# Kernel optimization log

Measured on AMD Instinct MI355X. Metric: run time of the kernel, lower is better.

Reference implementation:

```python
import jax, jax.numpy as jnp
import numpy as np

D_MODEL = 2048
NUM_HEADS = 16
HEAD_DIM = D_MODEL // NUM_HEADS  # 128; scale uses head_dim even though attention is over full d_model
B, S = 2, 2048


def setup_inputs() -> dict:
    key = jax.random.key(0)
    ks = jax.random.split(key, 5)
    x = jax.random.normal(ks[0], (B, S, D_MODEL), dtype=jnp.float32)
    # causal additive mask, as typically passed to this module (2D, sliced mask[-s:, :kv])
    neg = jnp.float32(-1e9)
    mask = jnp.where(jnp.triu(jnp.ones((S, S), dtype=bool), k=1), neg, jnp.float32(0.0))
    std = 1.0 / np.sqrt(D_MODEL)
    Wq = jax.random.normal(ks[1], (D_MODEL, D_MODEL), dtype=jnp.float32) * std
    Wk = jax.random.normal(ks[2], (D_MODEL, D_MODEL), dtype=jnp.float32) * std
    Wv = jax.random.normal(ks[3], (D_MODEL, D_MODEL), dtype=jnp.float32) * std
    Wo = jax.random.normal(ks[4], (D_MODEL, D_MODEL), dtype=jnp.float32) * std
    return {"x": x, "mask": mask, "Wq": Wq, "Wk": Wk, "Wv": Wv, "Wo": Wo}


def reference(x, mask, Wq, Wk, Wv, Wo):
    # nn.Linear(bias=False): y = x @ W^T
    q = jnp.einsum('bsd,ed->bse', x, Wq)  # [B,S,D]
    k = jnp.einsum('bsd,ed->bse', x, Wk)
    v = jnp.einsum('bsd,ed->bse', x, Wv)
    scale = jnp.float32(HEAD_DIM ** -0.5)
    # NOTE: faithful to source — contraction over full d_model, no head split
    scores = jnp.einsum('bsd,btd->bst', q, k) * scale  # [B,S,S]
    scores = scores + mask  # mask[-s:, :kv] == mask here (s == kv)
    weights = jax.nn.softmax(scores, axis=-1)
    out = jnp.einsum('bst,btd->bsd', weights, v)
    return jnp.einsum('bsd,ed->bse', out, Wo)
```

## Files before the change

### kernel.cpp

```cpp
#include <hip/hip_runtime.h>

#define DM  2048
#define SQ  2048
#define NB  2
#define BSZ (NB * SQ)

typedef _Float16 f16x8 __attribute__((ext_vector_type(8)));
typedef __attribute__((ext_vector_type(4))) float f32x4;

#define ASG(p) (const __attribute__((address_space(1))) void*)(p)
#define ASL(p) (__attribute__((address_space(3))) void*)(p)

__device__ __forceinline__ unsigned short f2h(float f) {
  union { _Float16 h; unsigned short u; } x;
  x.h = (_Float16)f;
  return x.u;
}

__global__ __launch_bounds__(256) void cast_f32(const float4* __restrict__ in,
                                                ushort4* __restrict__ out,
                                                int n4) {
  int i = blockIdx.x * 256 + threadIdx.x;
  if (i >= n4) return;
  float4 v = in[i];
  ushort4 h;
  h.x = f2h(v.x); h.y = f2h(v.y); h.z = f2h(v.z); h.w = f2h(v.w);
  out[i] = h;
}

#define SBAR8() do { \
    __builtin_amdgcn_sched_barrier(0); \
    __builtin_amdgcn_s_barrier(); \
    __builtin_amdgcn_sched_barrier(0); \
  } while (0)

#define STAGE8(BUFL, HALF, T) do { \
    const unsigned short* G_ = ((HALF) < 2) ? Ab : Bb; \
    const int ldG_ = ((HALF) < 2) ? ldA : ldB; \
    const int r0_ = (((HALF) < 2) ? bm0 : bn0) + ((HALF) & 1) * 128; \
    const long k0_ = (long)((T) << 6); \
    char* db_ = ldsb + (BUFL) * 65536 + (HALF) * 16384 + tid * 16; \
    const unsigned short* s0_ = G_ + (long)(r0_ + srow) * ldG_ + k0_ + scsw; \
    const unsigned short* s1_ = G_ + (long)(r0_ + 64 + srow) * ldG_ + k0_ + scsw; \
    __builtin_amdgcn_global_load_lds(ASG(s0_), ASL(db_), 16, 0, 0); \
    __builtin_amdgcn_global_load_lds(ASG(s1_), ASL(db_ + 8192), 16, 0, 0); \
  } while (0)

#define LDA8(BUFL, MQ, Af) do { \
    const char* ba_ = ldsb + (BUFL) * 65536 + wm * 16384 + (MQ) * 8192 + arow; \
    _Pragma("unroll") for (int mm_ = 0; mm_ < 4; mm_++) { \
      Af[mm_][0] = *(const f16x8*)(ba_ + mm_ * 2048 + sl0); \
      Af[mm_][1] = *(const f16x8*)(ba_ + mm_ * 2048 + sl1); } \
  } while (0)

#define LDB8(BUFL, NQ, Bf) do { \
    const char* bb_ = ldsb + (BUFL) * 65536 + 32768 + (wn * 2 + (NQ)) * 4096 + arow; \
    _Pragma("unroll") for (int nn_ = 0; nn_ < 2; nn_++) { \
      Bf[nn_][0] = *(const f16x8*)(bb_ + nn_ * 2048 + sl0); \
      Bf[nn_][1] = *(const f16x8*)(bb_ + nn_ * 2048 + sl1); } \
  } while (0)

#define PH8(Af, Bf, MQ, NQ) do { \
    __builtin_amdgcn_s_setprio(1); \
    _Pragma("unroll") for (int mm_ = 0; mm_ < 4; mm_++) \
    _Pragma("unroll") for (int nn_ = 0; nn_ < 2; nn_++) \
    _Pragma("unroll") for (int ks_ = 0; ks_ < 2; ks_++) \
      acc[(MQ) * 4 + mm_][(NQ) * 2 + nn_] = __builtin_amdgcn_mfma_f32_16x16x32_f16( \
          Af[mm_][ks_], Bf[nn_][ks_], acc[(MQ) * 4 + mm_][(NQ) * 2 + nn_], 0, 0, 0); \
    __builtin_amdgcn_s_setprio(0); \
  } while (0)

#define GROUP8(BUFL, T) do { \
    LDA8(BUFL, 0, a0); LDB8(BUFL, 0, b0); \
    if ((T) + 1 < NT) STAGE8(BUFL ^ 1, 3, (T) + 1); \
    SBAR8(); PH8(a0, b0, 0, 0); SBAR8(); \
    LDA8(BUFL, 1, a1); \
    SBAR8(); PH8(a1, b0, 1, 0); SBAR8(); \
    LDB8(BUFL, 1, b1); \
    if ((T) + 2 < NT) STAGE8(BUFL, 0, (T) + 2); \
    SBAR8(); PH8(a1, b1, 1, 1); SBAR8(); \
    if ((T) + 2 < NT) { STAGE8(BUFL, 1, (T) + 2); STAGE8(BUFL, 2, (T) + 2); } \
    SBAR8(); PH8(a0, b1, 0, 1); \
    __builtin_amdgcn_sched_barrier(0); \
    if ((T) + 1 < NT) { \
      if ((T) + 1 == NT - 1) { asm volatile("s_waitcnt vmcnt(0)" ::: "memory"); } \
      else                   { asm volatile("s_waitcnt vmcnt(6)" ::: "memory"); } \
    } \
    __builtin_amdgcn_s_barrier(); \
    __builtin_amdgcn_sched_barrier(0); \
  } while (0)

template <int OM>
__global__ __launch_bounds__(512, 2) void gemm8p(
    const unsigned short* __restrict__ A, const unsigned short* __restrict__ B,
    float* __restrict__ Cf, unsigned short* __restrict__ Ch,
    int K, int ldA, int ldB, int ldC) {
  __shared__ __align__(16) char ldsarr[131072];
  char* ldsb = ldsarr;

  const int bm0 = blockIdx.x * 256;
  const int bn0 = blockIdx.y * 256;
  const unsigned short* Ab = A;
  const unsigned short* Bb = B;

  const int tid = threadIdx.x, lane = tid & 63, wid = tid >> 6;
  const int wm = wid >> 2, wn = wid & 3;
  const int fr = lane & 15, fq = lane >> 4;
  const int NT = K >> 6;

  const int sl0 = ((fq ^ (fr & 7)) << 4);
  const int sl1 = (((4 + fq) ^ (fr & 7)) << 4);
  const int arow = fr << 7;

  const int srow = tid >> 3;
  const int scsw = ((tid & 7) ^ (srow & 7)) << 3;

  f32x4 acc[8][4];
#pragma unroll
  for (int m = 0; m < 8; m++)
#pragma unroll
    for (int n = 0; n < 4; n++)
#pragma unroll
      for (int r = 0; r < 4; r++) acc[m][n][r] = 0.f;

  f16x8 a0[4][2], a1[4][2], b0[2][2], b1[2][2];

  STAGE8(0, 0, 0); STAGE8(0, 1, 0); STAGE8(0, 2, 0); STAGE8(0, 3, 0);
  STAGE8(1, 0, 1); STAGE8(1, 1, 1); STAGE8(1, 2, 1);
  asm volatile("s_waitcnt vmcnt(6)" ::: "memory");
  __builtin_amdgcn_s_barrier();
  __builtin_amdgcn_sched_barrier(0);

  for (int t = 0; t < NT; t += 2) {
    GROUP8(0, t);
    GROUP8(1, t + 1);
  }

#pragma unroll
  for (int mq = 0; mq < 2; mq++)
#pragma unroll
    for (int mm = 0; mm < 4; mm++)
#pragma unroll
      for (int nq = 0; nq < 2; nq++)
#pragma unroll
        for (int nn = 0; nn < 2; nn++) {
          const int col = bn0 + wn * 64 + nq * 32 + nn * 16 + fr;
#pragma unroll
          for (int r = 0; r < 4; r++) {
            const long row = (long)bm0 + wm * 128 + mq * 64 + mm * 16 + fq * 4 + r;
            const long ci = row * ldC + col;
            if constexpr (OM == 0) Cf[ci] = acc[mq * 4 + mm][nq * 2 + nn][r];
            else                   Ch[ci] = f2h(acc[mq * 4 + mm][nq * 2 + nn][r]);
          }
        }
}

#define STAGER(BUFL, REG, U, T) do { \
    const unsigned short* G_ = (REG) ? Bb : Ab; \
    const int ldG_ = (REG) ? ldB : ldA; \
    const int r0_ = ((REG) ? bn0 : bm0) + (U) * 64; \
    const long k0_ = (long)((T) << 6); \
    char* db_ = ldsb + (BUFL) * 49152 + (REG) * 16384 + (U) * 8192 + tid * 16; \
    const unsigned short* s_ = G_ + (long)(r0_ + srow) * ldG_ + k0_ + scsw; \
    __builtin_amdgcn_global_load_lds(ASG(s_), ASL(db_), 16, 0, 0); \
  } while (0)

#define LDAR(BUFL, MH, Af) do { \
    const char* ba_ = ldsb + (BUFL) * 49152 + (wm * 64 + (MH) * 32) * 128 + arow; \
    _Pragma("unroll") for (int mm_ = 0; mm_ < 2; mm_++) { \
      Af[mm_][0] = *(const f16x8*)(ba_ + mm_ * 2048 + sl0); \
      Af[mm_][1] = *(const f16x8*)(ba_ + mm_ * 2048 + sl1); } \
  } while (0)

#define LDBR(BUFL, NH, Bf) do { \
    const char* bb_ = ldsb + (BUFL) * 49152 + 16384 + (wn * 64 + (NH) * 32) * 128 + arow; \
    _Pragma("unroll") for (int nn_ = 0; nn_ < 2; nn_++) { \
      Bf[nn_][0] = *(const f16x8*)(bb_ + nn_ * 2048 + sl0); \
      Bf[nn_][1] = *(const f16x8*)(bb_ + nn_ * 2048 + sl1); } \
  } while (0)

#define PHR(Af, Bf, MH, NH) do { \
    __builtin_amdgcn_s_setprio(1); \
    _Pragma("unroll") for (int mm_ = 0; mm_ < 2; mm_++) \
    _Pragma("unroll") for (int nn_ = 0; nn_ < 2; nn_++) \
    _Pragma("unroll") for (int ks_ = 0; ks_ < 2; ks_++) \
      acc[(MH) * 2 + mm_][(NH) * 2 + nn_] = __builtin_amdgcn_mfma_f32_16x16x32_f16( \
          Af[mm_][ks_], Bf[nn_][ks_], acc[(MH) * 2 + mm_][(NH) * 2 + nn_], 0, 0, 0); \
    __builtin_amdgcn_s_setprio(0); \
  } while (0)

#define GROUPR(BUFL, T) do { \
    LDAR(BUFL, 0, a0); LDBR(BUFL, 0, b0); \
    if ((T) + 1 < NT) STAGER(BUFL ^ 1, 1, 3, (T) + 1); \
    SBAR8(); PHR(a0, b0, 0, 0); SBAR8(); \
    LDAR(BUFL, 1, a1); \
    SBAR8(); PHR(a1, b0, 1, 0); SBAR8(); \
    LDBR(BUFL, 1, b1); \
    if ((T) + 2 < NT) { STAGER(BUFL, 0, 0, (T) + 2); STAGER(BUFL, 0, 1, (T) + 2); } \
    SBAR8(); PHR(a1, b1, 1, 1); SBAR8(); \
    if ((T) + 2 < NT) { STAGER(BUFL, 1, 0, (T) + 2); STAGER(BUFL, 1, 1, (T) + 2); STAGER(BUFL, 1, 2, (T) + 2); } \
    SBAR8(); PHR(a0, b1, 0, 1); \
    __builtin_amdgcn_sched_barrier(0); \
    if ((T) + 1 < NT) { \
      if ((T) + 1 == NT - 1) { asm volatile("s_waitcnt vmcnt(0)" ::: "memory"); } \
      else                   { asm volatile("s_waitcnt vmcnt(5)" ::: "memory"); } \
    } \
    __builtin_amdgcn_s_barrier(); \
    __builtin_amdgcn_sched_barrier(0); \
  } while (0)

template <int OM, int CAUSAL>
__global__ __launch_bounds__(512, 2) void gemm8pR(
    const unsigned short* __restrict__ A, const unsigned short* __restrict__ B,
    float* __restrict__ Cf, unsigned short* __restrict__ Ch,
    int K, long sAb, long sBb, long sCb,
    int ldA, int ldB, int ldC, float alpha) {
  __shared__ __align__(16) char ldsarr[98304];
  char* ldsb = ldsarr;

  const int bm0 = blockIdx.x * 128;
  const int bn0 = blockIdx.y * 256;
  if (CAUSAL == 1 && bn0 > bm0 + 127) return;

  const int z = blockIdx.z;
  const unsigned short* Ab = A + (long)z * sAb;
  const unsigned short* Bb = B + (long)z * sBb;
  const long cb = (long)z * sCb;

  const int tid = threadIdx.x, lane = tid & 63, wid = tid >> 6;
  const int wm = wid >> 2, wn = wid & 3;
  const int fr = lane & 15, fq = lane >> 4;
  int NT = K >> 6;
  if (CAUSAL == 2) NT = (bm0 + 128) >> 6;

  const int sl0 = ((fq ^ (fr & 7)) << 4);
  const int sl1 = (((4 + fq) ^ (fr & 7)) << 4);
  const int arow = fr << 7;

  const int srow = tid >> 3;
  const int scsw = ((tid & 7) ^ (srow & 7)) << 3;

  f32x4 acc[4][4];
#pragma unroll
  for (int m = 0; m < 4; m++)
#pragma unroll
    for (int n = 0; n < 4; n++)
#pragma unroll
      for (int r = 0; r < 4; r++) acc[m][n][r] = 0.f;

  f16x8 a0[2][2], a1[2][2], b0[2][2], b1[2][2];

  STAGER(0, 0, 0, 0); STAGER(0, 0, 1, 0);
  STAGER(0, 1, 0, 0); STAGER(0, 1, 1, 0); STAGER(0, 1, 2, 0); STAGER(0, 1, 3, 0);
  STAGER(1, 0, 0, 1); STAGER(1, 0, 1, 1);
  STAGER(1, 1, 0, 1); STAGER(1, 1, 1, 1); STAGER(1, 1, 2, 1);
  asm volatile("s_waitcnt vmcnt(5)" ::: "memory");
  __builtin_amdgcn_s_barrier();
  __builtin_amdgcn_sched_barrier(0);

  for (int t = 0; t < NT; t += 2) {
    GROUPR(0, t);
    GROUPR(1, t + 1);
  }

#pragma unroll
  for (int mh = 0; mh < 2; mh++)
#pragma unroll
    for (int mm = 0; mm < 2; mm++)
#pragma unroll
      for (int nh = 0; nh < 2; nh++)
#pragma unroll
        for (int nn = 0; nn < 2; nn++) {
          const int col = bn0 + wn * 64 + nh * 32 + nn * 16 + fr;
#pragma unroll
          for (int r = 0; r < 4; r++) {
            const long row = (long)bm0 + wm * 64 + mh * 32 + mm * 16 + fq * 4 + r;
            const long ci = cb + row * ldC + col;
            const float vv = acc[mh * 2 + mm][nh * 2 + nn][r] * alpha;
            if constexpr (OM == 0) Cf[ci] = vv;
            else                   Ch[ci] = f2h(vv);
          }
        }
}

__global__ __launch_bounds__(256) void softmax_causal(const float* __restrict__ sc,
                                                      unsigned short* __restrict__ pr) {
  const int row = blockIdx.x;
  const int s = row & (SQ - 1);
  const long base = (long)row * SQ;
  const int n = s + 1;
  const int tid = threadIdx.x;
  const int lane = tid & 63;
  const int wv = tid >> 6;
  __shared__ float red[4];

  float v[8];
  float mx = -3.0e38f;
#pragma unroll
  for (int j = 0; j < 8; j++) {
    const int i = tid + j * 256;
    v[j] = (i < n) ? sc[base + i] : -3.0e38f;
    mx = fmaxf(mx, v[j]);
  }
#pragma unroll
  for (int o = 32; o >= 1; o >>= 1) mx = fmaxf(mx, __shfl_xor(mx, o));
  if (lane == 0) red[wv] = mx;
  __syncthreads();
  mx = fmaxf(fmaxf(red[0], red[1]), fmaxf(red[2], red[3]));
  __syncthreads();

  float sum = 0.f;
#pragma unroll
  for (int j = 0; j < 8; j++) {
    const int i = tid + j * 256;
    v[j] = (i < n) ? __expf(v[j] - mx) : 0.f;
    sum += v[j];
  }
#pragma unroll
  for (int o = 32; o >= 1; o >>= 1) sum += __shfl_xor(sum, o);
  if (lane == 0) red[wv] = sum;
  __syncthreads();
  const float inv = 1.f / (red[0] + red[1] + red[2] + red[3]);
#pragma unroll
  for (int j = 0; j < 8; j++) {
    const int i = tid + j * 256;
    pr[base + i] = (i < n) ? f2h(v[j] * inv) : (unsigned short)0;
  }
}

extern "C" void kernel_launch(void* const* d_in, const int* in_sizes, int n_in,
                              void* d_out, int out_size, void* d_ws, size_t ws_size,
                              hipStream_t stream) {
  (void)in_sizes; (void)n_in; (void)out_size; (void)ws_size;
  const float* x  = (const float*)d_in[0];
  const float* Wq = (const float*)d_in[2];
  const float* Wk = (const float*)d_in[3];
  const float* Wv = (const float*)d_in[4];
  const float* Wo = (const float*)d_in[5];
  float* out = (float*)d_out;

  const long ELx = (long)BSZ * DM;
  const long ELw = (long)DM * DM;

  char* ws = (char*)d_ws;
  size_t off = 0;
  auto take = [&](size_t bytes) { void* p = ws + off; off += bytes; return p; };

  unsigned short* x16   = (unsigned short*)take(ELx * 2);
  unsigned short* wqk16 = (unsigned short*)take(2 * ELw * 2);
  unsigned short* wv16  = (unsigned short*)take(ELw * 2);
  unsigned short* wo16  = (unsigned short*)take(ELw * 2);
  unsigned short* qk16  = (unsigned short*)take((long)BSZ * 2 * DM * 2);
  unsigned short* vTT   = (unsigned short*)take(ELx * 2);
  unsigned short* probs = (unsigned short*)take((long)NB * SQ * SQ * 2);
  float* scores = (float*)ws;
  unsigned short* ctx = qk16;
  unsigned short* q16 = qk16;
  unsigned short* k16 = qk16 + DM;

  const int n4x = (int)(ELx / 4), n4w = (int)(ELw / 4);
  cast_f32<<<dim3(n4x / 256), 256, 0, stream>>>((const float4*)x,  (ushort4*)x16,        n4x);
  cast_f32<<<dim3(n4w / 256), 256, 0, stream>>>((const float4*)Wq, (ushort4*)wqk16,      n4w);
  cast_f32<<<dim3(n4w / 256), 256, 0, stream>>>((const float4*)Wk, (ushort4*)(wqk16 + ELw), n4w);
  cast_f32<<<dim3(n4w / 256), 256, 0, stream>>>((const float4*)Wv, (ushort4*)wv16,       n4w);
  cast_f32<<<dim3(n4w / 256), 256, 0, stream>>>((const float4*)Wo, (ushort4*)wo16,       n4w);

  const float scale = 0.08838834764831845f;

  gemm8p<1><<<dim3(BSZ / 256, 2 * DM / 256), 512, 0, stream>>>(
      x16, wqk16, nullptr, qk16, DM, DM, DM, 2 * DM);
  gemm8pR<1, 0><<<dim3(DM / 128, BSZ / 256, 1), 512, 0, stream>>>(
      wv16, x16, nullptr, vTT, DM, 0L, 0L, 0L, DM, DM, BSZ, 1.0f);
  gemm8pR<0, 1><<<dim3(SQ / 128, SQ / 256, NB), 512, 0, stream>>>(
      q16, k16, scores, nullptr, DM, (long)SQ * 2 * DM, (long)SQ * 2 * DM,
      (long)SQ * SQ, 2 * DM, 2 * DM, SQ, scale);

  softmax_causal<<<dim3(NB * SQ), 256, 0, stream>>>(scores, probs);

  gemm8pR<1, 2><<<dim3(SQ / 128, DM / 256, NB), 512, 0, stream>>>(
      probs, vTT, nullptr, ctx, SQ, (long)SQ * SQ, 2048L, (long)SQ * DM,
      SQ, BSZ, DM, 1.0f);
  gemm8pR<0, 0><<<dim3(BSZ / 128, DM / 256, 1), 512, 0, stream>>>(
      ctx, wo16, out, nullptr, DM, 0L, 0L, 0L, DM, DM, DM, 1.0f);
}
```

Baseline: 252.3 us.

## Drop redundant barriers in GEMM main loops and fuse weight cast kernels

Measured after the change: 240.8 us. 4.6% less time.

```diff
diff --git a/kernel.cpp b/kernel.cpp
--- a/kernel.cpp
+++ b/kernel.cpp
@@ -28,6 +28,22 @@
   out[i] = h;
 }
 
+__global__ __launch_bounds__(256) void cast_w4(const float4* __restrict__ a,
+                                               const float4* __restrict__ b,
+                                               const float4* __restrict__ c,
+                                               const float4* __restrict__ d,
+                                               ushort4* __restrict__ out,
+                                               int n4per) {
+  int i = blockIdx.x * 256 + threadIdx.x;
+  int seg = i / n4per, j = i - seg * n4per;
+  const float4* src = (seg == 0) ? a : (seg == 1) ? b : (seg == 2) ? c : d;
+  float4 v = src[j];
+  ushort4 h;
+  h.x = f2h(v.x); h.y = f2h(v.y); h.z = f2h(v.z); h.w = f2h(v.w);
+  out[i] = h;
+}
+
+#define SB() __builtin_amdgcn_sched_barrier(0)
 #define SBAR8() do { \
     __builtin_amdgcn_sched_barrier(0); \
     __builtin_amdgcn_s_barrier(); \
@@ -72,22 +88,31 @@
 
 #define GROUP8(BUFL, T) do { \
     LDA8(BUFL, 0, a0); LDB8(BUFL, 0, b0); \
+    SB(); \
+    LDA8(BUFL, 1, a1); \
+    SB(); \
     if ((T) + 1 < NT) STAGE8(BUFL ^ 1, 3, (T) + 1); \
-    SBAR8(); PH8(a0, b0, 0, 0); SBAR8(); \
-    LDA8(BUFL, 1, a1); \
-    SBAR8(); PH8(a1, b0, 1, 0); SBAR8(); \
+    SB(); \
+    PH8(a0, b0, 0, 0); \
+    SBAR8(); \
     LDB8(BUFL, 1, b1); \
+    SB(); \
+    PH8(a1, b0, 1, 0); \
+    SBAR8(); \
     if ((T) + 2 < NT) STAGE8(BUFL, 0, (T) + 2); \
-    SBAR8(); PH8(a1, b1, 1, 1); SBAR8(); \
+    SB(); \
+    PH8(a1, b1, 1, 1); \
+    SBAR8(); \
     if ((T) + 2 < NT) { STAGE8(BUFL, 1, (T) + 2); STAGE8(BUFL, 2, (T) + 2); } \
-    SBAR8(); PH8(a0, b1, 0, 1); \
-    __builtin_amdgcn_sched_barrier(0); \
+    SB(); \
+    PH8(a0, b1, 0, 1); \
+    SB(); \
     if ((T) + 1 < NT) { \
       if ((T) + 1 == NT - 1) { asm volatile("s_waitcnt vmcnt(0)" ::: "memory"); } \
       else                   { asm volatile("s_waitcnt vmcnt(6)" ::: "memory"); } \
     } \
     __builtin_amdgcn_s_barrier(); \
-    __builtin_amdgcn_sched_barrier(0); \
+    SB(); \
   } while (0)
 
 template <int OM>
@@ -129,7 +154,7 @@
   STAGE8(1, 0, 1); STAGE8(1, 1, 1); STAGE8(1, 2, 1);
   asm volatile("s_waitcnt vmcnt(6)" ::: "memory");
   __builtin_amdgcn_s_barrier();
-  __builtin_amdgcn_sched_barrier(0);
+  SB();
 
   for (int t = 0; t < NT; t += 2) {
     GROUP8(0, t);
@@ -191,22 +216,31 @@
 
 #define GROUPR(BUFL, T) do { \
     LDAR(BUFL, 0, a0); LDBR(BUFL, 0, b0); \
+    SB(); \
+    LDAR(BUFL, 1, a1); \
+    SB(); \
     if ((T) + 1 < NT) STAGER(BUFL ^ 1, 1, 3, (T) + 1); \
-    SBAR8(); PHR(a0, b0, 0, 0); SBAR8(); \
-    LDAR(BUFL, 1, a1); \
-    SBAR8(); PHR(a1, b0, 1, 0); SBAR8(); \
+    SB(); \
+    PHR(a0, b0, 0, 0); \
+    SBAR8(); \
     LDBR(BUFL, 1, b1); \
+    SB(); \
+    PHR(a1, b0, 1, 0); \
+    SBAR8(); \
     if ((T) + 2 < NT) { STAGER(BUFL, 0, 0, (T) + 2); STAGER(BUFL, 0, 1, (T) + 2); } \
-    SBAR8(); PHR(a1, b1, 1, 1); SBAR8(); \
+    SB(); \
+    PHR(a1, b1, 1, 1); \
+    SBAR8(); \
     if ((T) + 2 < NT) { STAGER(BUFL, 1, 0, (T) + 2); STAGER(BUFL, 1, 1, (T) + 2); STAGER(BUFL, 1, 2, (T) + 2); } \
-    SBAR8(); PHR(a0, b1, 0, 1); \
-    __builtin_amdgcn_sched_barrier(0); \
+    SB(); \
+    PHR(a0, b1, 0, 1); \
+    SB(); \
     if ((T) + 1 < NT) { \
       if ((T) + 1 == NT - 1) { asm volatile("s_waitcnt vmcnt(0)" ::: "memory"); } \
       else                   { asm volatile("s_waitcnt vmcnt(5)" ::: "memory"); } \
     } \
     __builtin_amdgcn_s_barrier(); \
-    __builtin_amdgcn_sched_barrier(0); \
+    SB(); \
   } while (0)
 
 template <int OM, int CAUSAL>
@@ -256,7 +290,7 @@
   STAGER(1, 1, 0, 1); STAGER(1, 1, 1, 1); STAGER(1, 1, 2, 1);
   asm volatile("s_waitcnt vmcnt(5)" ::: "memory");
   __builtin_amdgcn_s_barrier();
-  __builtin_amdgcn_sched_barrier(0);
+  SB();
 
   for (int t = 0; t < NT; t += 2) {
     GROUPR(0, t);
@@ -359,11 +393,10 @@
   unsigned short* k16 = qk16 + DM;
 
   const int n4x = (int)(ELx / 4), n4w = (int)(ELw / 4);
-  cast_f32<<<dim3(n4x / 256), 256, 0, stream>>>((const float4*)x,  (ushort4*)x16,        n4x);
-  cast_f32<<<dim3(n4w / 256), 256, 0, stream>>>((const float4*)Wq, (ushort4*)wqk16,      n4w);
-  cast_f32<<<dim3(n4w / 256), 256, 0, stream>>>((const float4*)Wk, (ushort4*)(wqk16 + ELw), n4w);
-  cast_f32<<<dim3(n4w / 256), 256, 0, stream>>>((const float4*)Wv, (ushort4*)wv16,       n4w);
-  cast_f32<<<dim3(n4w / 256), 256, 0, stream>>>((const float4*)Wo, (ushort4*)wo16,       n4w);
+  cast_f32<<<dim3(n4x / 256), 256, 0, stream>>>((const float4*)x, (ushort4*)x16, n4x);
+  cast_w4<<<dim3(4 * n4w / 256), 256, 0, stream>>>(
+      (const float4*)Wq, (const float4*)Wk, (const float4*)Wv, (const float4*)Wo,
+      (ushort4*)wqk16, n4w);
 
   const float scale = 0.08838834764831845f;
 
```
